# Kernel tuning notes

Measured on AMD Instinct MI355X. Metric: run time of the kernel, lower is better.

Reference implementation:

```python
import jax, jax.numpy as jnp
from jax import lax
import numpy as np

B, S, E, HID = 16, 7, 64, 64
RES = (64, 64); D = RES[0] * RES[1]
XLOW, XHIGH = -0.5, 0.5
RLOW, RHIGH = float(np.sqrt(0.01)), float(np.sqrt(0.05))
PIXEL_MULT = 1.0; N_ITER = 3; TSOFT = 1.0 / float(np.sqrt(E))

def _build_grid():
    ranges = [np.linspace(XLOW, XHIGH, r) for r in RES]
    g = np.stack(np.meshgrid(*ranges, indexing='xy'), axis=-1)
    g = g.reshape(RES[0], RES[1], -1).reshape(1, -1, 2)
    return jnp.asarray(g, dtype=jnp.float32)

ABS_GRID = _build_grid()  # [1, D, 2]

def _ln(x, g, b):
    m = jnp.mean(x, -1, keepdims=True)
    v = jnp.mean(jnp.square(x - m), -1, keepdims=True)
    return (x - m) * lax.rsqrt(v + 1e-5) * g + b

def _forward(data, slot_noise, pos_rand, conv0_w, conv0_b, conv1_w, conv1_b, conv2_w, conv2_b,
             dataN_g, dataN_b, queryN_g, queryN_b, toK_w, toK_b, toV_w, toV_b, dense_w, dense_b,
             mlp1_w, mlp1_b, mlp2_w, mlp2_b, gru_wih, gru_whh, gru_bih, gru_bhh,
             alpha1_w, alpha1_b, alpha2_w, alpha2_b, final1_w, final1_b, final2_w, final2_b,
             slots_mu, slots_logsigma):
    dn = ('NCHW', 'OIHW', 'NCHW')
    def conv(x, w, b):
        return lax.conv_general_dilated(x, w, (1, 1), 'SAME', dimension_numbers=dn) + b[None, :, None, None]
    # CNN encoder: Conv-ReLU x3, 'same' padding, k=5
    x = jax.nn.relu(conv(data, conv0_w, conv0_b))
    x = jax.nn.relu(conv(x, conv1_w, conv1_b))
    x = jax.nn.relu(conv(x, conv2_w, conv2_b))
    enc = x.transpose(0, 2, 3, 1).reshape(B, D, HID)
    enc = _ln(enc, dataN_g, dataN_b)

    queries = slots_mu + jnp.exp(slots_logsigma) * slot_noise  # [B,S,E]
    # init_slots: faithful replication (source indexes the SLOT dim, and swaps rlow/rhigh)
    pos_scale = pos_rand.at[:, :2, :].add(-0.5)
    pos_scale = pos_scale.at[:, -1, :].set((RLOW - RHIGH) * pos_rand[:, -1, :] + RHIGH)

    encK = enc @ toK_w + toK_b  # [B,D,E]
    encV = enc @ toV_w + toV_b

    def init_mlp(y):
        y = _ln(y, queryN_g, queryN_b)
        return jax.nn.relu(y @ mlp1_w + mlp1_b) @ mlp2_w + mlp2_b

    def get_kv(ps):
        # per-slot relative grid: [B,S,D,2]
        rel = (ABS_GRID[:, None] - ps[:, :, None, :2]) / ps[:, :, -1][:, :, None, None]
        eg = PIXEL_MULT * (rel @ dense_w + dense_b)  # [B,S,D,E]
        return init_mlp(encK[:, None] + eg), init_mlp(encV[:, None] + eg)

    def att_wts(q, k):
        logits = jnp.einsum('bse,bsde->bsd', q, k) * TSOFT
        att = jax.nn.softmax(logits, axis=1)  # softmax over slots
        wts = att / jnp.sum(att, -1, keepdims=True) + 1e-8
        return att, wts

    def update_frames(wts):
        new_pos = jnp.einsum('bsd,de->bse', wts, ABS_GRID[0])  # [B,S,2]
        d2 = jnp.sum(jnp.square(ABS_GRID[:, None] - new_pos[:, :, None]), -1)  # [B,S,D]
        new_scale = jnp.sqrt(jnp.einsum('bsd,bsd->bs', wts, d2))
        return jnp.concatenate([new_pos, new_scale[..., None]], -1)

    def gru(xg, h):
        gi = xg @ gru_wih.T + gru_bih
        gh = h @ gru_whh.T + gru_bhh
        ir, iz, inn = jnp.split(gi, 3, -1)
        hr, hz, hn = jnp.split(gh, 3, -1)
        r = jax.nn.sigmoid(ir + hr)
        z = jax.nn.sigmoid(iz + hz)
        n = jnp.tanh(inn + r * hn)
        return (1.0 - z) * n + z * h

    for _ in range(N_ITER):
        keys, vals = get_kv(pos_scale)
        att, wts = att_wts(_ln(queries, queryN_g, queryN_b), keys)
        pos_scale = update_frames(wts)
        upd = jnp.einsum('bsd,bsde->bse', wts, vals)
        queries = gru(upd.reshape(-1, E), queries.reshape(-1, E)).reshape(B, S, E)

    keys, _ = get_kv(pos_scale)
    att, wts = att_wts(_ln(queries, queryN_g, queryN_b), keys)
    nps = update_frames(wts)
    alpha = jax.nn.sigmoid(jax.nn.relu(queries @ alpha1_w + alpha1_b) @ alpha2_w + alpha2_b)
    slot_feat = jax.nn.relu(queries @ final1_w + final1_b) @ final2_w + final2_b + nps
    return queries, att, slot_feat, alpha

def setup_inputs() -> dict:
    ks = jax.random.split(jax.random.key(0), 20)
    f32 = jnp.float32
    def rn(i, shape, s):
        return jax.random.normal(ks[i], shape, f32) * s
    inp = dict(
        data=jax.random.normal(ks[0], (B, 1, RES[0], RES[1]), f32),
        slot_noise=jax.random.normal(ks[1], (B, S, E), f32),
        pos_rand=jax.random.uniform(ks[2], (B, S, 3), dtype=f32),
        conv0_w=rn(3, (HID, 1, 5, 5), 0.2), conv0_b=jnp.zeros(HID, f32),
        conv1_w=rn(4, (HID, HID, 5, 5), 0.025), conv1_b=jnp.zeros(HID, f32),
        conv2_w=rn(5, (HID, HID, 5, 5), 0.025), conv2_b=jnp.zeros(HID, f32),
        dataN_g=jnp.ones(HID, f32), dataN_b=jnp.zeros(HID, f32),
        queryN_g=jnp.ones(E, f32), queryN_b=jnp.zeros(E, f32),
        toK_w=rn(6, (HID, E), 0.125), toK_b=jnp.zeros(E, f32),
        toV_w=rn(7, (HID, E), 0.125), toV_b=jnp.zeros(E, f32),
        dense_w=rn(8, (2, E), 0.7), dense_b=jnp.zeros(E, f32),
        mlp1_w=rn(9, (E, E), 0.125), mlp1_b=jnp.zeros(E, f32),
        mlp2_w=rn(10, (E, E), 0.125), mlp2_b=jnp.zeros(E, f32),
        gru_wih=rn(11, (3 * E, E), 0.125), gru_whh=rn(12, (3 * E, E), 0.125),
        gru_bih=jnp.zeros(3 * E, f32), gru_bhh=jnp.zeros(3 * E, f32),
        alpha1_w=rn(13, (E, 32), 0.125), alpha1_b=jnp.zeros(32, f32),
        alpha2_w=rn(14, (32, 1), 0.18), alpha2_b=jnp.zeros(1, f32),
        final1_w=rn(15, (E, HID), 0.125), final1_b=jnp.zeros(HID, f32),
        final2_w=rn(16, (HID, 3), 0.125), final2_b=jnp.zeros(3, f32),
        slots_mu=rn(17, (1, 1, E), 1.0),
        slots_logsigma=rn(18, (1, 1, E), 0.01),
    )
    return inp

def reference(data, slot_noise, pos_rand, conv0_w, conv0_b, conv1_w, conv1_b, conv2_w, conv2_b,
              dataN_g, dataN_b, queryN_g, queryN_b, toK_w, toK_b, toV_w, toV_b, dense_w, dense_b,
              mlp1_w, mlp1_b, mlp2_w, mlp2_b, gru_wih, gru_whh, gru_bih, gru_bhh,
              alpha1_w, alpha1_b, alpha2_w, alpha2_b, final1_w, final1_b, final2_w, final2_b,
              slots_mu, slots_logsigma):
    return _forward(data, slot_noise, pos_rand, conv0_w, conv0_b, conv1_w, conv1_b, conv2_w, conv2_b,
                    dataN_g, dataN_b, queryN_g, queryN_b, toK_w, toK_b, toV_w, toV_b, dense_w, dense_b,
                    mlp1_w, mlp1_b, mlp2_w, mlp2_b, gru_wih, gru_whh, gru_bih, gru_bhh,
                    alpha1_w, alpha1_b, alpha2_w, alpha2_b, final1_w, final1_b, final2_w, final2_b,
                    slots_mu, slots_logsigma)
```

## Files before the change

kernel.cpp:

```cpp
#include <hip/hip_runtime.h>
#include <cmath>


#define RLOW_F 0.1f
#define RHIGH_F 0.22360679774997896f
#define W0CONST 1.00004096f
#define SR2 704.3386243f

typedef __attribute__((ext_vector_type(8))) __bf16 bf16x8;
typedef __attribute__((ext_vector_type(4))) float f32x4;

__device__ __forceinline__ float wsum64(float v){
  #pragma unroll
  for (int off = 32; off > 0; off >>= 1) v += __shfl_xor(v, off, 64);
  return v;
}
__device__ __forceinline__ float rdlane(float v, int l){
  return __int_as_float(__builtin_amdgcn_readlane(__float_as_int(v), l));
}
__device__ __forceinline__ unsigned short bf16bits(float v){
  __bf16 h = (__bf16)v;
  return *reinterpret_cast<unsigned short*>(&h);
}

__device__ __forceinline__ void pp_core(int row, int e, float qv,
    float px, float py, float sc,
    const float* __restrict__ qg_, const float* __restrict__ qb_,
    const float* __restrict__ dw, const float* __restrict__ db,
    const float* __restrict__ mlp2w, const float* __restrict__ mlp2b,
    float* __restrict__ absc, float* __restrict__ w2qc){
  float m = wsum64(qv) * (1.f/64.f);
  float d = qv - m;
  float var = wsum64(d*d) * (1.f/64.f);
  float qlnv = d * (1.0f/sqrtf(var + 1e-5f)) * qg_[e] + qb_[e];
  float A  = dw[e]      / sc;
  float Bv = dw[64 + e] / sc;
  absc[row*192 + e]       = A;
  absc[row*192 + 64 + e]  = Bv;
  absc[row*192 + 128 + e] = db[e] - px*A - py*Bv;
  float acc = 0.f;
  const float* wrow = mlp2w + e*64;
  for (int j = 0; j < 64; j++) acc = fmaf(wrow[j], rdlane(qlnv, j), acc);
  w2qc[row*68 + e] = acc;
  float c2 = wsum64(mlp2b[e] * qlnv);
  if (e == 0) w2qc[row*68 + 64] = c2;
}

__global__ void k_prep(const float* __restrict__ noise, const float* __restrict__ prand,
                       const float* __restrict__ mu, const float* __restrict__ logsig,
                       const float* __restrict__ qg_, const float* __restrict__ qb_,
                       const float* __restrict__ dw, const float* __restrict__ db,
                       const float* __restrict__ mlp2w, const float* __restrict__ mlp2b,
                       float* __restrict__ queries, float* __restrict__ ps,
                       float* __restrict__ absc, float* __restrict__ w2qc,
                       float* __restrict__ accF, float* __restrict__ upd){
  int row = blockIdx.x;
  int e = threadIdx.x;
  int s = row % 7;
  float qv = mu[e] + expf(logsig[e]) * noise[row*64 + e];
  queries[row*64 + e] = qv;
  upd[row*64 + e] = 0.f;
  if (e < 4) accF[row*4 + e] = 0.f;
  float pv = 0.f;
  if (e < 3){
    float pr = prand[row*3 + e];
    if (s < 2)       pv = pr - 0.5f;
    else if (s == 6) pv = (RLOW_F - RHIGH_F)*pr + RHIGH_F;
    else             pv = pr;
    ps[row*3 + e] = pv;
  }
  float px = rdlane(pv, 0), py = rdlane(pv, 1), sc = rdlane(pv, 2);
  pp_core(row, e, qv, px, py, sc, qg_, qb_, dw, db, mlp2w, mlp2b, absc, w2qc);
}

__global__ __launch_bounds__(256) void k_conv0(const float* __restrict__ in,
                        const float* __restrict__ w, const float* __restrict__ bias,
                        unsigned short* __restrict__ out){
  int bi = blockIdx.x; int b = bi >> 6; int y = bi & 63;
  int t = threadIdx.x; int lane = t & 63; int xg = t >> 6;
  __shared__ float s_in[5*68];
  __shared__ float s_w[64*25];
  __shared__ float s_out[64*65];
  for (int i = t; i < 1600; i += 256) s_w[i] = w[i];
  for (int i = t; i < 340; i += 256){
    int r = i / 68, cx = i % 68;
    int yy = y + r - 2, gx = cx - 2;
    float v = 0.f;
    if (yy >= 0 && yy < 64 && gx >= 0 && gx < 64) v = in[(b*64 + yy)*64 + gx];
    s_in[r*68 + cx] = v;
  }
  __syncthreads();
  int o = lane;
  float bvv = bias[o];
  float acc[16];
  #pragma unroll
  for (int k = 0; k < 16; k++) acc[k] = bvv;
  #pragma unroll
  for (int ky = 0; ky < 5; ky++){
    float rv[20];
    const float4* p = reinterpret_cast<const float4*>(&s_in[ky*68 + xg*16]);
    #pragma unroll
    for (int q = 0; q < 5; q++){ float4 f = p[q]; rv[q*4]=f.x; rv[q*4+1]=f.y; rv[q*4+2]=f.z; rv[q*4+3]=f.w; }
    #pragma unroll
    for (int kx = 0; kx < 5; kx++){
      float wv = s_w[o*25 + ky*5 + kx];
      #pragma unroll
      for (int k = 0; k < 16; k++) acc[k] = fmaf(rv[k+kx], wv, acc[k]);
    }
  }
  #pragma unroll
  for (int k = 0; k < 16; k++) s_out[o*65 + xg*16 + k] = fmaxf(acc[k], 0.f);
  __syncthreads();
  for (int i = t; i < 4096; i += 256){
    int px = i >> 6, ch = i & 63;
    out[((size_t)(b*64 + y)*64 + px)*64 + ch] = bf16bits(s_out[ch*65 + px]);
  }
}

__global__ void k_packconv(const float* __restrict__ w, unsigned short* __restrict__ out){
  int idx = blockIdx.x*256 + threadIdx.x;
  if (idx >= 102400) return;
  int j = idx & 7;
  int l = (idx >> 3) & 63;
  int frag = idx >> 9;
  int nt = frag & 3;
  int ks = (frag >> 2) % 10;
  int dy = frag / 40;
  int q = l >> 4, cr = l & 15;
  int k = ks*32 + q*8 + j;
  int kx = k >> 6, ch = k & 63;
  int n = nt*16 + cr;
  out[idx] = bf16bits(w[((n*64 + ch)*5 + dy)*5 + kx]);
}

__global__ __launch_bounds__(256) void k_convm(const unsigned short* __restrict__ in_bf,
                        const unsigned short* __restrict__ wpack,
                        const float* __restrict__ bias,
                        const float* __restrict__ lng, const float* __restrict__ lnb,
                        unsigned short* __restrict__ out_bf, float* __restrict__ out_f,
                        int mode){
  int bi = blockIdx.x;
  int b = bi >> 4; int yg = bi & 15;
  int t = threadIdx.x; int wv = t >> 6; int l = t & 63;
  int q = l >> 4, cr = l & 15;
  int p0 = wv*16;

  __shared__ char lds[8*68*144];

  for (int ri = 0; ri < 8; ri++){
    int yy = yg*4 + ri - 2;
    bool rok = (yy >= 0 && yy < 64);
    const uint4* src = reinterpret_cast<const uint4*>(in_bf + (size_t)(b*64 + yy)*64*64);
    for (int i = t; i < 544; i += 256){
      int px = i >> 3, c8 = i & 7;
      uint4 v = {0u,0u,0u,0u};
      int gx = px - 2;
      if (rok && gx >= 0 && gx < 64) v = src[gx*8 + c8];
      *reinterpret_cast<uint4*>(&lds[ri*9792 + px*144 + c8*16]) = v;
    }
  }
  __syncthreads();

  f32x4 acc[4][4];
  #pragma unroll
  for (int r = 0; r < 4; r++)
    #pragma unroll
    for (int nt = 0; nt < 4; nt++) acc[r][nt] = (f32x4){0.f,0.f,0.f,0.f};

  const bf16x8* wp = reinterpret_cast<const bf16x8*>(wpack);
  for (int dy = 0; dy < 5; dy++){
    for (int ks = 0; ks < 10; ks++){
      bf16x8 Bf[4];
      int fbase = (dy*10 + ks)*4;
      #pragma unroll
      for (int nt = 0; nt < 4; nt++) Bf[nt] = wp[(fbase + nt)*64 + l];
      int aoff = (p0 + cr + (ks >> 1))*144 + (ks & 1)*64 + q*16;
      #pragma unroll
      for (int r = 0; r < 4; r++){
        bf16x8 a = *reinterpret_cast<const bf16x8*>(&lds[(r + dy)*9792 + aoff]);
        #pragma unroll
        for (int nt = 0; nt < 4; nt++)
          acc[r][nt] = __builtin_amdgcn_mfma_f32_16x16x32_bf16(a, Bf[nt], acc[r][nt], 0, 0, 0);
      }
    }
  }

  float bvv[4];
  #pragma unroll
  for (int nt = 0; nt < 4; nt++) bvv[nt] = bias[nt*16 + cr];

  if (mode == 0){
    #pragma unroll
    for (int r = 0; r < 4; r++){
      int y = yg*4 + r;
      #pragma unroll
      for (int reg = 0; reg < 4; reg++){
        int p = p0 + q*4 + reg;
        size_t base = ((size_t)(b*64 + y)*64 + p)*64;
        #pragma unroll
        for (int nt = 0; nt < 4; nt++)
          out_bf[base + nt*16 + cr] = bf16bits(fmaxf(acc[r][nt][reg] + bvv[nt], 0.f));
      }
    }
  } else {
    float gv[4], bb[4];
    #pragma unroll
    for (int nt = 0; nt < 4; nt++){ gv[nt] = lng[nt*16 + cr]; bb[nt] = lnb[nt*16 + cr]; }
    #pragma unroll
    for (int r = 0; r < 4; r++){
      int y = yg*4 + r;
      #pragma unroll
      for (int reg = 0; reg < 4; reg++){
        int p = p0 + q*4 + reg;
        float v[4]; float s1 = 0.f, s2 = 0.f;
        #pragma unroll
        for (int nt = 0; nt < 4; nt++){
          v[nt] = fmaxf(acc[r][nt][reg] + bvv[nt], 0.f);
          s1 += v[nt]; s2 += v[nt]*v[nt];
        }
        #pragma unroll
        for (int m = 1; m < 16; m <<= 1){ s1 += __shfl_xor(s1, m, 64); s2 += __shfl_xor(s2, m, 64); }
        float mean = s1 * (1.f/64.f);
        float var  = s2 * (1.f/64.f) - mean*mean;
        float rstd = 1.0f/sqrtf(var + 1e-5f);
        size_t base = ((size_t)b*4096 + y*64 + p)*64;
        #pragma unroll
        for (int nt = 0; nt < 4; nt++)
          out_f[base + nt*16 + cr] = (v[nt] - mean)*rstd*gv[nt] + bb[nt];
      }
    }
  }
}

__global__ void k_packw1(const float* __restrict__ w1, unsigned short* __restrict__ out){
  int idx = blockIdx.x*256 + threadIdx.x;
  int jj = idx & 7;
  int lane = (idx >> 3) & 63;
  int frag = idx >> 9;
  int ks = frag >> 2, nt = frag & 3;
  int q = lane >> 4, cr = lane & 15;
  int k = ks*32 + q*8 + jj;
  int n = nt*16 + cr;
  out[idx] = bf16bits(w1[k*64 + n]);
}

__global__ __launch_bounds__(256) void k_projm(const float* __restrict__ enc,
                       const unsigned short* __restrict__ kpack, const float* __restrict__ bk,
                       const unsigned short* __restrict__ vpack, const float* __restrict__ bvp,
                       unsigned short* __restrict__ K, unsigned short* __restrict__ V){
  int bi = blockIdx.x; int b = bi >> 6; int tile = bi & 63;
  int t = threadIdx.x; int wv = t >> 6; int l = t & 63;
  int q = l >> 4, cr = l & 15;
  int d0 = tile*64 + wv*16;

  const bf16x8* kp = reinterpret_cast<const bf16x8*>(kpack);
  const bf16x8* vp = reinterpret_cast<const bf16x8*>(vpack);
  bf16x8 KB[8], VB[8];
  #pragma unroll
  for (int f = 0; f < 8; f++){ KB[f] = kp[f*64 + l]; VB[f] = vp[f*64 + l]; }

  const float* er = enc + (size_t)(b*4096 + d0 + cr)*64;
  bf16x8 a0, a1;
  #pragma unroll
  for (int h = 0; h < 2; h++){
    const float4* e4 = reinterpret_cast<const float4*>(er + (h ? (32 + q*8) : (q*8)));
    #pragma unroll
    for (int p = 0; p < 2; p++){
      float4 e = e4[p];
      if (h == 0){ a0[p*4+0]=(__bf16)e.x; a0[p*4+1]=(__bf16)e.y; a0[p*4+2]=(__bf16)e.z; a0[p*4+3]=(__bf16)e.w; }
      else       { a1[p*4+0]=(__bf16)e.x; a1[p*4+1]=(__bf16)e.y; a1[p*4+2]=(__bf16)e.z; a1[p*4+3]=(__bf16)e.w; }
    }
  }

  f32x4 zero = {0.f,0.f,0.f,0.f};
  f32x4 aK[4], aV[4];
  #pragma unroll
  for (int nt = 0; nt < 4; nt++){
    aK[nt] = __builtin_amdgcn_mfma_f32_16x16x32_bf16(a0, KB[nt],     zero,   0, 0, 0);
    aK[nt] = __builtin_amdgcn_mfma_f32_16x16x32_bf16(a1, KB[4 + nt], aK[nt], 0, 0, 0);
    aV[nt] = __builtin_amdgcn_mfma_f32_16x16x32_bf16(a0, VB[nt],     zero,   0, 0, 0);
    aV[nt] = __builtin_amdgcn_mfma_f32_16x16x32_bf16(a1, VB[4 + nt], aV[nt], 0, 0, 0);
  }
  #pragma unroll
  for (int nt = 0; nt < 4; nt++){
    float bkv = bk[nt*16 + cr], bvv = bvp[nt*16 + cr];
    #pragma unroll
    for (int reg = 0; reg < 4; reg++){
      size_t base = ((size_t)b*4096 + d0 + q*4 + reg)*64 + nt*16 + cr;
      K[base] = bf16bits(aK[nt][reg] + bkv);
      V[base] = bf16bits(aV[nt][reg] + bvv);
    }
  }
}

__global__ __launch_bounds__(256) void k_attnK(const unsigned short* __restrict__ encX,
     const unsigned short* __restrict__ w1pack, const float* __restrict__ mlp1b,
     const float* __restrict__ absc, const float* __restrict__ qg_,
     const float* __restrict__ qb_, const float* __restrict__ w2qc,
     float* __restrict__ att, float* __restrict__ accF){
  int bi = blockIdx.x;
  int b = bi >> 6, tile = bi & 63;
  int t = threadIdx.x; int wv = t >> 6; int l = t & 63;
  int q = l >> 4, cr = l & 15;
  int m0 = tile*64 + wv*16;
  int drow = m0 + cr;

  __shared__ float s_log[7*64];
  __shared__ float s_absc[7*192];
  __shared__ float s_wq[7*68];
  for (int i = t; i < 1344; i += 256) s_absc[i] = absc[b*7*192 + i];
  for (int i = t; i < 476;  i += 256) s_wq[i]   = w2qc[b*7*68 + i];

  const bf16x8* wp = reinterpret_cast<const bf16x8*>(w1pack);
  bf16x8 Bf[8];
  #pragma unroll
  for (int f = 0; f < 8; f++) Bf[f] = wp[f*64 + l];

  const unsigned short* er = encX + (size_t)(b*4096 + drow)*64;
  float gx = -0.5f + (float)(drow & 63) * (1.f/63.f);
  float gy = -0.5f + (float)((drow >> 6) & 63) * (1.f/63.f);
  float xb[16], gq[16], bq[16];
  {
    bf16x8 ea = *reinterpret_cast<const bf16x8*>(er + q*8);
    bf16x8 eb = *reinterpret_cast<const bf16x8*>(er + 32 + q*8);
    #pragma unroll
    for (int i = 0; i < 8; i++){ xb[i] = (float)ea[i]; xb[8+i] = (float)eb[i]; }
  }
  #pragma unroll
  for (int h = 0; h < 2; h++){
    int fb = h ? (32 + q*8) : (q*8);
    const float4* g4 = reinterpret_cast<const float4*>(qg_ + fb);
    const float4* b4 = reinterpret_cast<const float4*>(qb_ + fb);
    #pragma unroll
    for (int p = 0; p < 2; p++){
      float4 gg = g4[p], bb = b4[p];
      int o = h*8 + p*4;
      gq[o+0]=gg.x; gq[o+1]=gg.y; gq[o+2]=gg.z; gq[o+3]=gg.w;
      bq[o+0]=bb.x; bq[o+1]=bb.y; bq[o+2]=bb.z; bq[o+3]=bb.w;
    }
  }
  float b1v[4];
  #pragma unroll
  for (int nt = 0; nt < 4; nt++) b1v[nt] = mlp1b[nt*16 + cr];
  __syncthreads();

  for (int s = 0; s < 7; s++){
    const float* Ac = s_absc + s*192;
    float x[16];
    #pragma unroll
    for (int h = 0; h < 2; h++){
      int fb = h ? (32 + q*8) : (q*8);
      const float4* A4 = reinterpret_cast<const float4*>(Ac + fb);
      const float4* B4 = reinterpret_cast<const float4*>(Ac + 64 + fb);
      const float4* C4 = reinterpret_cast<const float4*>(Ac + 128 + fb);
      #pragma unroll
      for (int p = 0; p < 2; p++){
        float4 Av = A4[p], Bv = B4[p], Cv = C4[p];
        int o = h*8 + p*4;
        x[o+0] = xb[o+0] + gx*Av.x + gy*Bv.x + Cv.x;
        x[o+1] = xb[o+1] + gx*Av.y + gy*Bv.y + Cv.y;
        x[o+2] = xb[o+2] + gx*Av.z + gy*Bv.z + Cv.z;
        x[o+3] = xb[o+3] + gx*Av.w + gy*Bv.w + Cv.w;
      }
    }
    float sum = 0.f;
    #pragma unroll
    for (int k = 0; k < 16; k++) sum += x[k];
    sum += __shfl_xor(sum, 16, 64); sum += __shfl_xor(sum, 32, 64);
    float m = sum * (1.f/64.f);
    float v = 0.f;
    #pragma unroll
    for (int k = 0; k < 16; k++){ float dd = x[k] - m; v += dd*dd; }
    v += __shfl_xor(v, 16, 64); v += __shfl_xor(v, 32, 64);
    float rstd = 1.0f/sqrtf(v * (1.f/64.f) + 1e-5f);

    bf16x8 a0, a1;
    #pragma unroll
    for (int k = 0; k < 8; k++)  a0[k] = (__bf16)((x[k]   - m)*rstd*gq[k]   + bq[k]);
    #pragma unroll
    for (int k = 0; k < 8; k++)  a1[k] = (__bf16)((x[8+k] - m)*rstd*gq[8+k] + bq[8+k]);

    f32x4 zero = {0.f, 0.f, 0.f, 0.f};
    f32x4 acc[4];
    #pragma unroll
    for (int nt = 0; nt < 4; nt++){
      acc[nt] = __builtin_amdgcn_mfma_f32_16x16x32_bf16(a0, Bf[nt],     zero,    0, 0, 0);
      acc[nt] = __builtin_amdgcn_mfma_f32_16x16x32_bf16(a1, Bf[4 + nt], acc[nt], 0, 0, 0);
    }

    float c2 = s_wq[s*68 + 64];
    float p[4] = {0.f, 0.f, 0.f, 0.f};
    #pragma unroll
    for (int nt = 0; nt < 4; nt++){
      float wqv = s_wq[s*68 + nt*16 + cr];
      #pragma unroll
      for (int reg = 0; reg < 4; reg++){
        float y = fmaxf(acc[nt][reg] + b1v[nt], 0.f);
        p[reg] = fmaf(y, wqv, p[reg]);
      }
    }
    #pragma unroll
    for (int reg = 0; reg < 4; reg++){
      #pragma unroll
      for (int off = 1; off < 16; off <<= 1) p[reg] += __shfl_xor(p[reg], off, 64);
    }
    if (cr == 0){
      #pragma unroll
      for (int reg = 0; reg < 4; reg++)
        s_log[s*64 + wv*16 + q*4 + reg] = (p[reg] + c2) * 0.125f;
    }
  }
  __syncthreads();

  if (t < 64){
    float lv[7];
    #pragma unroll
    for (int s = 0; s < 7; s++) lv[s] = s_log[s*64 + t];
    float mx = lv[0];
    #pragma unroll
    for (int s = 1; s < 7; s++) mx = fmaxf(mx, lv[s]);
    float sm = 0.f;
    #pragma unroll
    for (int s = 0; s < 7; s++){ lv[s] = expf(lv[s] - mx); sm += lv[s]; }
    float inv = 1.0f / sm;
    #pragma unroll
    for (int s = 0; s < 7; s++){
      float a = lv[s] * inv;
      s_log[s*64 + t] = a;
      att[(size_t)(b*7+s)*4096 + tile*64 + t] = a;
    }
  }
  __syncthreads();

  if (t < 224){
    int s = t >> 5, r = t & 31;
    float a1 = s_log[s*64 + r];
    float a2 = s_log[s*64 + r + 32];
    float gx1 = -0.5f + (float)r * (1.f/63.f);
    float gx2 = -0.5f + (float)(r + 32) * (1.f/63.f);
    float gyc = -0.5f + (float)tile * (1.f/63.f);
    float gy2c = gyc*gyc;
    float w0 = a1 + a2;
    float w1 = a1*gx1 + a2*gx2;
    float w2 = w0*gyc;
    float w3 = a1*(gx1*gx1 + gy2c) + a2*(gx2*gx2 + gy2c);
    #pragma unroll
    for (int m = 1; m < 32; m <<= 1){
      w0 += __shfl_xor(w0, m, 64);
      w1 += __shfl_xor(w1, m, 64);
      w2 += __shfl_xor(w2, m, 64);
      w3 += __shfl_xor(w3, m, 64);
    }
    if (r == 0){
      atomicAdd(&accF[(b*7+s)*4 + 0], w0);
      atomicAdd(&accF[(b*7+s)*4 + 1], w1);
      atomicAdd(&accF[(b*7+s)*4 + 2], w2);
      atomicAdd(&accF[(b*7+s)*4 + 3], w3);
    }
  }
}

__global__ __launch_bounds__(256) void k_attnV(const unsigned short* __restrict__ encX,
     const unsigned short* __restrict__ w1pack, const float* __restrict__ mlp1b,
     const float* __restrict__ absc, const float* __restrict__ qg_,
     const float* __restrict__ qb_, const float* __restrict__ att,
     const float* __restrict__ accF, float* __restrict__ upd){
  int bi = blockIdx.x;
  int b = bi >> 6, tile = bi & 63;
  int t = threadIdx.x; int wv = t >> 6; int l = t & 63;
  int q = l >> 4, cr = l & 15;
  int m0 = tile*64 + wv*16;
  int drow = m0 + cr;

  __shared__ float s_absc[7*192];
  __shared__ float s_att[7*64];
  __shared__ float s_upd[7*64];
  __shared__ float s_inv[7];
  for (int i = t; i < 1344; i += 256) s_absc[i] = absc[b*7*192 + i];
  for (int i = t; i < 448;  i += 256){
    s_att[i] = att[(size_t)(b*7 + (i >> 6))*4096 + tile*64 + (i & 63)];
    s_upd[i] = 0.f;
  }
  if (t < 7) s_inv[t] = 1.0f / accF[(b*7 + t)*4];

  const bf16x8* wp = reinterpret_cast<const bf16x8*>(w1pack);
  bf16x8 Bf[8];
  #pragma unroll
  for (int f = 0; f < 8; f++) Bf[f] = wp[f*64 + l];

  const unsigned short* er = encX + (size_t)(b*4096 + drow)*64;
  float gx = -0.5f + (float)(drow & 63) * (1.f/63.f);
  float gy = -0.5f + (float)((drow >> 6) & 63) * (1.f/63.f);
  float xb[16], gq[16], bq[16];
  {
    bf16x8 ea = *reinterpret_cast<const bf16x8*>(er + q*8);
    bf16x8 eb = *reinterpret_cast<const bf16x8*>(er + 32 + q*8);
    #pragma unroll
    for (int i = 0; i < 8; i++){ xb[i] = (float)ea[i]; xb[8+i] = (float)eb[i]; }
  }
  #pragma unroll
  for (int h = 0; h < 2; h++){
    int fb = h ? (32 + q*8) : (q*8);
    const float4* g4 = reinterpret_cast<const float4*>(qg_ + fb);
    const float4* b4 = reinterpret_cast<const float4*>(qb_ + fb);
    #pragma unroll
    for (int p = 0; p < 2; p++){
      float4 gg = g4[p], bb = b4[p];
      int o = h*8 + p*4;
      gq[o+0]=gg.x; gq[o+1]=gg.y; gq[o+2]=gg.z; gq[o+3]=gg.w;
      bq[o+0]=bb.x; bq[o+1]=bb.y; bq[o+2]=bb.z; bq[o+3]=bb.w;
    }
  }
  float b1v[4];
  #pragma unroll
  for (int nt = 0; nt < 4; nt++) b1v[nt] = mlp1b[nt*16 + cr];
  __syncthreads();

  for (int s = 0; s < 7; s++){
    const float* Ac = s_absc + s*192;
    float x[16];
    #pragma unroll
    for (int h = 0; h < 2; h++){
      int fb = h ? (32 + q*8) : (q*8);
      const float4* A4 = reinterpret_cast<const float4*>(Ac + fb);
      const float4* B4 = reinterpret_cast<const float4*>(Ac + 64 + fb);
      const float4* C4 = reinterpret_cast<const float4*>(Ac + 128 + fb);
      #pragma unroll
      for (int p = 0; p < 2; p++){
        float4 Av = A4[p], Bv = B4[p], Cv = C4[p];
        int o = h*8 + p*4;
        x[o+0] = xb[o+0] + gx*Av.x + gy*Bv.x + Cv.x;
        x[o+1] = xb[o+1] + gx*Av.y + gy*Bv.y + Cv.y;
        x[o+2] = xb[o+2] + gx*Av.z + gy*Bv.z + Cv.z;
        x[o+3] = xb[o+3] + gx*Av.w + gy*Bv.w + Cv.w;
      }
    }
    float sum = 0.f;
    #pragma unroll
    for (int k = 0; k < 16; k++) sum += x[k];
    sum += __shfl_xor(sum, 16, 64); sum += __shfl_xor(sum, 32, 64);
    float m = sum * (1.f/64.f);
    float v = 0.f;
    #pragma unroll
    for (int k = 0; k < 16; k++){ float dd = x[k] - m; v += dd*dd; }
    v += __shfl_xor(v, 16, 64); v += __shfl_xor(v, 32, 64);
    float rstd = 1.0f/sqrtf(v * (1.f/64.f) + 1e-5f);

    bf16x8 a0, a1;
    #pragma unroll
    for (int k = 0; k < 8; k++)  a0[k] = (__bf16)((x[k]   - m)*rstd*gq[k]   + bq[k]);
    #pragma unroll
    for (int k = 0; k < 8; k++)  a1[k] = (__bf16)((x[8+k] - m)*rstd*gq[8+k] + bq[8+k]);

    f32x4 zero = {0.f, 0.f, 0.f, 0.f};
    f32x4 acc[4];
    #pragma unroll
    for (int nt = 0; nt < 4; nt++){
      acc[nt] = __builtin_amdgcn_mfma_f32_16x16x32_bf16(a0, Bf[nt],     zero,    0, 0, 0);
      acc[nt] = __builtin_amdgcn_mfma_f32_16x16x32_bf16(a1, Bf[4 + nt], acc[nt], 0, 0, 0);
    }

    float rsa = s_inv[s];
    float wr[4];
    #pragma unroll
    for (int reg = 0; reg < 4; reg++)
      wr[reg] = fmaf(s_att[s*64 + wv*16 + q*4 + reg], rsa, 1e-8f);
    float pc[4];
    #pragma unroll
    for (int nt = 0; nt < 4; nt++){
      pc[nt] = 0.f;
      #pragma unroll
      for (int reg = 0; reg < 4; reg++)
        pc[nt] = fmaf(wr[reg], fmaxf(acc[nt][reg] + b1v[nt], 0.f), pc[nt]);
    }
    #pragma unroll
    for (int nt = 0; nt < 4; nt++){
      pc[nt] += __shfl_xor(pc[nt], 16, 64);
      pc[nt] += __shfl_xor(pc[nt], 32, 64);
    }
    if (q == 0){
      #pragma unroll
      for (int nt = 0; nt < 4; nt++)
        atomicAdd(&s_upd[s*64 + nt*16 + cr], pc[nt]);
    }
  }
  __syncthreads();
  for (int i = t; i < 448; i += 256)
    atomicAdd(&upd[b*448 + i], s_upd[i]);
}

__global__ void k_gru(float* __restrict__ upd, float* __restrict__ queries,
                      const float* __restrict__ wih, const float* __restrict__ whh,
                      const float* __restrict__ bih, const float* __restrict__ bhh,
                      const float* __restrict__ mlp2w, const float* __restrict__ mlp2b,
                      float* __restrict__ accF, float* __restrict__ ps,
                      const float* __restrict__ qg_, const float* __restrict__ qb_,
                      const float* __restrict__ dw, const float* __restrict__ db,
                      float* __restrict__ absc, float* __restrict__ w2qc){
  int row = blockIdx.x; int t = threadIdx.x;
  __shared__ float us[64], hs[64], xs[64], gis[192], ghs[192];
  __shared__ float s_ps3[3];
  if (t < 64){ us[t] = upd[row*64 + t]; hs[t] = queries[row*64 + t]; }
  if (t == 64){
    float sa = accF[row*4+0];
    float ax = accF[row*4+1], ay = accF[row*4+2], ar2 = accF[row*4+3];
    float isa = 1.0f/sa;
    float Wx = ax*isa, Wy = ay*isa;
    float Wg = ar2*isa + 1e-8f*SR2;
    float s2 = Wg - (Wx*Wx + Wy*Wy)*(2.f - W0CONST);
    s_ps3[0] = Wx; s_ps3[1] = Wy; s_ps3[2] = sqrtf(fmaxf(s2, 0.f));
  }
  __syncthreads();
  if (t < 64){
    float a = W0CONST * mlp2b[t];
    for (int i = 0; i < 64; i++) a = fmaf(us[i], mlp2w[i*64 + t], a);
    xs[t] = a;
  }
  __syncthreads();
  float gi = bih[t], gh = bhh[t];
  for (int e = 0; e < 64; e++){
    gi = fmaf(wih[t*64 + e], xs[e], gi);
    gh = fmaf(whh[t*64 + e], hs[e], gh);
  }
  gis[t] = gi; ghs[t] = gh;
  __syncthreads();
  if (t < 64){
    float r = 1.0f/(1.0f + expf(-(gis[t]      + ghs[t])));
    float z = 1.0f/(1.0f + expf(-(gis[64+t]   + ghs[64+t])));
    float n = tanhf(gis[128+t] + r*ghs[128+t]);
    float newq = (1.0f - z)*n + z*hs[t];
    queries[row*64 + t] = newq;
    upd[row*64 + t] = 0.f;
    if (t < 4) accF[row*4 + t] = 0.f;
    if (t < 3) ps[row*3 + t] = s_ps3[t];
    pp_core(row, t, newq, s_ps3[0], s_ps3[1], s_ps3[2],
            qg_, qb_, dw, db, mlp2w, mlp2b, absc, w2qc);
  }
}

__global__ void k_final(const float* __restrict__ queries, const float* __restrict__ accF,
                        const float* __restrict__ a1w, const float* __restrict__ a1b,
                        const float* __restrict__ a2w, const float* __restrict__ a2b,
                        const float* __restrict__ f1w, const float* __restrict__ f1b,
                        const float* __restrict__ f2w, const float* __restrict__ f2b,
                        float* __restrict__ out){
  int bs = blockIdx.x; int e = threadIdx.x;
  __shared__ float qs[64], hf[64], ha[32];
  float q = queries[bs*64 + e];
  qs[e] = q;
  out[bs*64 + e] = q;
  __syncthreads();
  float accf = f1b[e];
  for (int i = 0; i < 64; i++) accf = fmaf(qs[i], f1w[i*64 + e], accf);
  hf[e] = fmaxf(accf, 0.f);
  if (e < 32){
    float acca = a1b[e];
    for (int i = 0; i < 64; i++) acca = fmaf(qs[i], a1w[i*32 + e], acca);
    ha[e] = fmaxf(acca, 0.f);
  }
  __syncthreads();
  if (e < 3){
    float sf = f2b[e];
    for (int o = 0; o < 64; o++) sf = fmaf(hf[o], f2w[o*3 + e], sf);
    float sa = accF[bs*4+0], ax = accF[bs*4+1], ay = accF[bs*4+2], ar2 = accF[bs*4+3];
    float isa = 1.0f/sa;
    float Wx = ax*isa, Wy = ay*isa;
    float Wg = ar2*isa + 1e-8f*SR2;
    float s2 = Wg - (Wx*Wx + Wy*Wy)*(2.f - W0CONST);
    float nv = (e == 0) ? Wx : ((e == 1) ? Wy : sqrtf(fmaxf(s2, 0.f)));
    out[465920 + bs*3 + e] = sf + nv;
  }
  if (e == 32){
    float al = a2b[0];
    for (int o = 0; o < 32; o++) al = fmaf(ha[o], a2w[o], al);
    out[466256 + bs] = 1.0f/(1.0f + expf(-al));
  }
}

extern "C" void kernel_launch(void* const* d_in, const int* in_sizes, int n_in,
                              void* d_out, int out_size, void* d_ws, size_t ws_size,
                              hipStream_t stream){
  const float* data        = (const float*)d_in[0];
  const float* slot_noise  = (const float*)d_in[1];
  const float* pos_rand    = (const float*)d_in[2];
  const float* conv0_w     = (const float*)d_in[3];
  const float* conv0_b     = (const float*)d_in[4];
  const float* conv1_w     = (const float*)d_in[5];
  const float* conv1_b     = (const float*)d_in[6];
  const float* conv2_w     = (const float*)d_in[7];
  const float* conv2_b     = (const float*)d_in[8];
  const float* dataN_g     = (const float*)d_in[9];
  const float* dataN_b     = (const float*)d_in[10];
  const float* queryN_g    = (const float*)d_in[11];
  const float* queryN_b    = (const float*)d_in[12];
  const float* toK_w       = (const float*)d_in[13];
  const float* toK_b       = (const float*)d_in[14];
  const float* toV_w       = (const float*)d_in[15];
  const float* toV_b       = (const float*)d_in[16];
  const float* dense_w     = (const float*)d_in[17];
  const float* dense_b     = (const float*)d_in[18];
  const float* mlp1_w      = (const float*)d_in[19];
  const float* mlp1_b      = (const float*)d_in[20];
  const float* mlp2_w      = (const float*)d_in[21];
  const float* mlp2_b      = (const float*)d_in[22];
  const float* gru_wih     = (const float*)d_in[23];
  const float* gru_whh     = (const float*)d_in[24];
  const float* gru_bih     = (const float*)d_in[25];
  const float* gru_bhh     = (const float*)d_in[26];
  const float* alpha1_w    = (const float*)d_in[27];
  const float* alpha1_b    = (const float*)d_in[28];
  const float* alpha2_w    = (const float*)d_in[29];
  const float* alpha2_b    = (const float*)d_in[30];
  const float* final1_w    = (const float*)d_in[31];
  const float* final1_b    = (const float*)d_in[32];
  const float* final2_w    = (const float*)d_in[33];
  const float* final2_b    = (const float*)d_in[34];
  const float* slots_mu    = (const float*)d_in[35];
  const float* slots_lsig  = (const float*)d_in[36];

  float* ws   = (float*)d_ws;
  float* bufA = ws;
  float* bufB = bufA + 4194304;
  float* bufC = bufB + 4194304;
  float* attw = bufC + 4194304;
  float* queries = attw + 458752;
  float* ps   = queries + 7168;
  float* absc = ps + 512;
  float* accF = absc + 21504;
  float* upd  = accF + 512;
  float* w2qc = upd + 7168;
  unsigned short* w1pack = (unsigned short*)(w2qc + 7616);
  unsigned short* kpack  = w1pack + 4096;
  unsigned short* vpack  = kpack + 4096;
  unsigned short* wp1    = vpack + 4096;
  unsigned short* wp2    = wp1 + 102400;

  unsigned short* c0_bf = (unsigned short*)bufA;
  unsigned short* c1_bf = (unsigned short*)bufC;
  float* enc = bufB;
  unsigned short* encK = (unsigned short*)bufA;
  unsigned short* encV = (unsigned short*)bufC;

  float* outq   = (float*)d_out;
  float* outatt = outq + 7168;

  k_prep<<<112, 64, 0, stream>>>(slot_noise, pos_rand, slots_mu, slots_lsig,
                                 queryN_g, queryN_b, dense_w, dense_b, mlp2_w, mlp2_b,
                                 queries, ps, absc, w2qc, accF, upd);
  k_packw1<<<16, 256, 0, stream>>>(mlp1_w, w1pack);
  k_packw1<<<16, 256, 0, stream>>>(toK_w, kpack);
  k_packw1<<<16, 256, 0, stream>>>(toV_w, vpack);
  k_packconv<<<400, 256, 0, stream>>>(conv1_w, wp1);
  k_packconv<<<400, 256, 0, stream>>>(conv2_w, wp2);
  k_conv0<<<1024, 256, 0, stream>>>(data, conv0_w, conv0_b, c0_bf);
  k_convm<<<256, 256, 0, stream>>>(c0_bf, wp1, conv1_b, nullptr, nullptr, c1_bf, nullptr, 0);
  k_convm<<<256, 256, 0, stream>>>(c1_bf, wp2, conv2_b, dataN_g, dataN_b, nullptr, enc, 1);
  k_projm<<<1024, 256, 0, stream>>>(enc, kpack, toK_b, vpack, toV_b, encK, encV);

  for (int p = 0; p < 4; p++){
    float* attp = (p == 3) ? outatt : attw;
    k_attnK<<<1024, 256, 0, stream>>>(encK, w1pack, mlp1_b, absc, queryN_g, queryN_b,
                                      w2qc, attp, accF);
    if (p < 3){
      k_attnV<<<1024, 256, 0, stream>>>(encV, w1pack, mlp1_b, absc, queryN_g, queryN_b,
                                        attp, accF, upd);
      k_gru<<<112, 192, 0, stream>>>(upd, queries, gru_wih, gru_whh, gru_bih, gru_bhh,
                                     mlp2_w, mlp2_b, accF, ps, queryN_g, queryN_b,
                                     dense_w, dense_b, absc, w2qc);
    }
  }
  k_final<<<112, 64, 0, stream>>>(queries, accF,
                                  alpha1_w, alpha1_b, alpha2_w, alpha2_b,
                                  final1_w, final1_b, final2_w, final2_b, outq);
}
```

Before: 535.2 us.

## Fuse attention-K and attention-V kernels with deferred normalization and partitioned accumulators

The separate key-logit and value-update kernels become one kernel. It computes the softmax attention per tile and, in the same launch, accumulates the weighted value MLP outputs. The per-slot attention normalization (divide by total attention mass) is moved into the GRU kernel by keeping two partial sums, the attention-weighted sum and the plain sum for the epsilon term. This removes the intermediate attention buffer round-trip and one launch per iteration. Tiles shrink to 32 rows, with slots split across wave pairs for more blocks, and global atomics are spread over 4 partition buffers to reduce contention. The cost is extra shared-memory atomics and partial-sum traffic.

```diff
diff --git a/kernel.cpp b/kernel.cpp
--- a/kernel.cpp
+++ b/kernel.cpp
@@ -53,14 +53,14 @@
                        const float* __restrict__ mlp2w, const float* __restrict__ mlp2b,
                        float* __restrict__ queries, float* __restrict__ ps,
                        float* __restrict__ absc, float* __restrict__ w2qc,
-                       float* __restrict__ accF, float* __restrict__ upd){
+                       float* __restrict__ accF, float* __restrict__ gpbuf){
   int row = blockIdx.x;
   int e = threadIdx.x;
   int s = row % 7;
   float qv = mu[e] + expf(logsig[e]) * noise[row*64 + e];
   queries[row*64 + e] = qv;
-  upd[row*64 + e] = 0.f;
   if (e < 4) accF[row*4 + e] = 0.f;
+  for (int i = row*64 + e; i < 57344; i += 7168) gpbuf[i] = 0.f;
   float pv = 0.f;
   if (e < 3){
     float pr = prand[row*3 + e];
@@ -293,39 +293,42 @@
   }
 }
 
-__global__ __launch_bounds__(256) void k_attnK(const unsigned short* __restrict__ encX,
+__global__ __launch_bounds__(256) void k_attn(
+     const unsigned short* __restrict__ encK, const unsigned short* __restrict__ encV,
      const unsigned short* __restrict__ w1pack, const float* __restrict__ mlp1b,
      const float* __restrict__ absc, const float* __restrict__ qg_,
      const float* __restrict__ qb_, const float* __restrict__ w2qc,
-     float* __restrict__ att, float* __restrict__ accF){
+     float* __restrict__ accF, float* __restrict__ gp1P, float* __restrict__ gp2P,
+     float* __restrict__ att_out, int mode){
   int bi = blockIdx.x;
-  int b = bi >> 6, tile = bi & 63;
+  int b = bi >> 7, tile = bi & 127;
   int t = threadIdx.x; int wv = t >> 6; int l = t & 63;
   int q = l >> 4, cr = l & 15;
-  int m0 = tile*64 + wv*16;
+  int rg = wv & 1, sg = wv >> 1;
+  int m0 = tile*32 + rg*16;
   int drow = m0 + cr;
-
-  __shared__ float s_log[7*64];
+  int sbeg = sg*4, send = sg ? 7 : 4;
+
+  __shared__ float s_log[7*32];
   __shared__ float s_absc[7*192];
   __shared__ float s_wq[7*68];
-  for (int i = t; i < 1344; i += 256) s_absc[i] = absc[b*7*192 + i];
-  for (int i = t; i < 476;  i += 256) s_wq[i]   = w2qc[b*7*68 + i];
+  __shared__ float s_up1[7*64];
+  __shared__ float s_up2[7*64];
+
+  for (int i = t; i < 1344; i += 256) s_absc[i] = absc[b*1344 + i];
+  for (int i = t; i < 476;  i += 256) s_wq[i]   = w2qc[b*476 + i];
+  if (mode == 0){
+    for (int i = t; i < 448; i += 256){ s_up1[i] = 0.f; s_up2[i] = 0.f; }
+  }
 
   const bf16x8* wp = reinterpret_cast<const bf16x8*>(w1pack);
   bf16x8 Bf[8];
   #pragma unroll
   for (int f = 0; f < 8; f++) Bf[f] = wp[f*64 + l];
 
-  const unsigned short* er = encX + (size_t)(b*4096 + drow)*64;
   float gx = -0.5f + (float)(drow & 63) * (1.f/63.f);
   float gy = -0.5f + (float)((drow >> 6) & 63) * (1.f/63.f);
-  float xb[16], gq[16], bq[16];
-  {
-    bf16x8 ea = *reinterpret_cast<const bf16x8*>(er + q*8);
-    bf16x8 eb = *reinterpret_cast<const bf16x8*>(er + 32 + q*8);
-    #pragma unroll
-    for (int i = 0; i < 8; i++){ xb[i] = (float)ea[i]; xb[8+i] = (float)eb[i]; }
-  }
+  float gq[16], bq[16];
   #pragma unroll
   for (int h = 0; h < 2; h++){
     int fb = h ? (32 + q*8) : (q*8);
@@ -342,9 +345,18 @@
   float b1v[4];
   #pragma unroll
   for (int nt = 0; nt < 4; nt++) b1v[nt] = mlp1b[nt*16 + cr];
-  __syncthreads();
-
-  for (int s = 0; s < 7; s++){
+
+  float xb[16];
+  {
+    const unsigned short* er = encK + (size_t)(b*4096 + drow)*64;
+    bf16x8 ea = *reinterpret_cast<const bf16x8*>(er + q*8);
+    bf16x8 eb = *reinterpret_cast<const bf16x8*>(er + 32 + q*8);
+    #pragma unroll
+    for (int i = 0; i < 8; i++){ xb[i] = (float)ea[i]; xb[8+i] = (float)eb[i]; }
+  }
+  __syncthreads();
+
+  for (int s = sbeg; s < send; s++){
     const float* Ac = s_absc + s*192;
     float x[16];
     #pragma unroll
@@ -407,15 +419,15 @@
     if (cr == 0){
       #pragma unroll
       for (int reg = 0; reg < 4; reg++)
-        s_log[s*64 + wv*16 + q*4 + reg] = (p[reg] + c2) * 0.125f;
-    }
-  }
-  __syncthreads();
-
-  if (t < 64){
+        s_log[s*32 + rg*16 + q*4 + reg] = (p[reg] + c2) * 0.125f;
+    }
+  }
+  __syncthreads();
+
+  if (t < 32){
     float lv[7];
     #pragma unroll
-    for (int s = 0; s < 7; s++) lv[s] = s_log[s*64 + t];
+    for (int s = 0; s < 7; s++) lv[s] = s_log[s*32 + t];
     float mx = lv[0];
     #pragma unroll
     for (int s = 1; s < 7; s++) mx = fmaxf(mx, lv[s]);
@@ -426,24 +438,19 @@
     #pragma unroll
     for (int s = 0; s < 7; s++){
       float a = lv[s] * inv;
-      s_log[s*64 + t] = a;
-      att[(size_t)(b*7+s)*4096 + tile*64 + t] = a;
+      s_log[s*32 + t] = a;
+      if (mode == 1) att_out[(size_t)(b*7+s)*4096 + tile*32 + t] = a;
     }
   }
   __syncthreads();
 
   if (t < 224){
     int s = t >> 5, r = t & 31;
-    float a1 = s_log[s*64 + r];
-    float a2 = s_log[s*64 + r + 32];
-    float gx1 = -0.5f + (float)r * (1.f/63.f);
-    float gx2 = -0.5f + (float)(r + 32) * (1.f/63.f);
-    float gyc = -0.5f + (float)tile * (1.f/63.f);
-    float gy2c = gyc*gyc;
-    float w0 = a1 + a2;
-    float w1 = a1*gx1 + a2*gx2;
-    float w2 = w0*gyc;
-    float w3 = a1*(gx1*gx1 + gy2c) + a2*(gx2*gx2 + gy2c);
+    float a = s_log[s*32 + r];
+    int d = tile*32 + r;
+    float gxr = -0.5f + (float)(d & 63) * (1.f/63.f);
+    float gyr = -0.5f + (float)(d >> 6) * (1.f/63.f);
+    float w0 = a, w1 = a*gxr, w2 = a*gyr, w3 = a*(gxr*gxr + gyr*gyr);
     #pragma unroll
     for (int m = 1; m < 32; m <<= 1){
       w0 += __shfl_xor(w0, m, 64);
@@ -458,138 +465,103 @@
       atomicAdd(&accF[(b*7+s)*4 + 3], w3);
     }
   }
-}
-
-__global__ __launch_bounds__(256) void k_attnV(const unsigned short* __restrict__ encX,
-     const unsigned short* __restrict__ w1pack, const float* __restrict__ mlp1b,
-     const float* __restrict__ absc, const float* __restrict__ qg_,
-     const float* __restrict__ qb_, const float* __restrict__ att,
-     const float* __restrict__ accF, float* __restrict__ upd){
-  int bi = blockIdx.x;
-  int b = bi >> 6, tile = bi & 63;
-  int t = threadIdx.x; int wv = t >> 6; int l = t & 63;
-  int q = l >> 4, cr = l & 15;
-  int m0 = tile*64 + wv*16;
-  int drow = m0 + cr;
-
-  __shared__ float s_absc[7*192];
-  __shared__ float s_att[7*64];
-  __shared__ float s_upd[7*64];
-  __shared__ float s_inv[7];
-  for (int i = t; i < 1344; i += 256) s_absc[i] = absc[b*7*192 + i];
-  for (int i = t; i < 448;  i += 256){
-    s_att[i] = att[(size_t)(b*7 + (i >> 6))*4096 + tile*64 + (i & 63)];
-    s_upd[i] = 0.f;
-  }
-  if (t < 7) s_inv[t] = 1.0f / accF[(b*7 + t)*4];
-
-  const bf16x8* wp = reinterpret_cast<const bf16x8*>(w1pack);
-  bf16x8 Bf[8];
-  #pragma unroll
-  for (int f = 0; f < 8; f++) Bf[f] = wp[f*64 + l];
-
-  const unsigned short* er = encX + (size_t)(b*4096 + drow)*64;
-  float gx = -0.5f + (float)(drow & 63) * (1.f/63.f);
-  float gy = -0.5f + (float)((drow >> 6) & 63) * (1.f/63.f);
-  float xb[16], gq[16], bq[16];
-  {
-    bf16x8 ea = *reinterpret_cast<const bf16x8*>(er + q*8);
-    bf16x8 eb = *reinterpret_cast<const bf16x8*>(er + 32 + q*8);
-    #pragma unroll
-    for (int i = 0; i < 8; i++){ xb[i] = (float)ea[i]; xb[8+i] = (float)eb[i]; }
-  }
-  #pragma unroll
-  for (int h = 0; h < 2; h++){
-    int fb = h ? (32 + q*8) : (q*8);
-    const float4* g4 = reinterpret_cast<const float4*>(qg_ + fb);
-    const float4* b4 = reinterpret_cast<const float4*>(qb_ + fb);
-    #pragma unroll
-    for (int p = 0; p < 2; p++){
-      float4 gg = g4[p], bb = b4[p];
-      int o = h*8 + p*4;
-      gq[o+0]=gg.x; gq[o+1]=gg.y; gq[o+2]=gg.z; gq[o+3]=gg.w;
-      bq[o+0]=bb.x; bq[o+1]=bb.y; bq[o+2]=bb.z; bq[o+3]=bb.w;
-    }
-  }
-  float b1v[4];
-  #pragma unroll
-  for (int nt = 0; nt < 4; nt++) b1v[nt] = mlp1b[nt*16 + cr];
-  __syncthreads();
-
-  for (int s = 0; s < 7; s++){
-    const float* Ac = s_absc + s*192;
-    float x[16];
-    #pragma unroll
-    for (int h = 0; h < 2; h++){
-      int fb = h ? (32 + q*8) : (q*8);
-      const float4* A4 = reinterpret_cast<const float4*>(Ac + fb);
-      const float4* B4 = reinterpret_cast<const float4*>(Ac + 64 + fb);
-      const float4* C4 = reinterpret_cast<const float4*>(Ac + 128 + fb);
-      #pragma unroll
-      for (int p = 0; p < 2; p++){
-        float4 Av = A4[p], Bv = B4[p], Cv = C4[p];
-        int o = h*8 + p*4;
-        x[o+0] = xb[o+0] + gx*Av.x + gy*Bv.x + Cv.x;
-        x[o+1] = xb[o+1] + gx*Av.y + gy*Bv.y + Cv.y;
-        x[o+2] = xb[o+2] + gx*Av.z + gy*Bv.z + Cv.z;
-        x[o+3] = xb[o+3] + gx*Av.w + gy*Bv.w + Cv.w;
-      }
-    }
-    float sum = 0.f;
-    #pragma unroll
-    for (int k = 0; k < 16; k++) sum += x[k];
-    sum += __shfl_xor(sum, 16, 64); sum += __shfl_xor(sum, 32, 64);
-    float m = sum * (1.f/64.f);
-    float v = 0.f;
-    #pragma unroll
-    for (int k = 0; k < 16; k++){ float dd = x[k] - m; v += dd*dd; }
-    v += __shfl_xor(v, 16, 64); v += __shfl_xor(v, 32, 64);
-    float rstd = 1.0f/sqrtf(v * (1.f/64.f) + 1e-5f);
-
-    bf16x8 a0, a1;
-    #pragma unroll
-    for (int k = 0; k < 8; k++)  a0[k] = (__bf16)((x[k]   - m)*rstd*gq[k]   + bq[k]);
-    #pragma unroll
-    for (int k = 0; k < 8; k++)  a1[k] = (__bf16)((x[8+k] - m)*rstd*gq[8+k] + bq[8+k]);
-
-    f32x4 zero = {0.f, 0.f, 0.f, 0.f};
-    f32x4 acc[4];
-    #pragma unroll
-    for (int nt = 0; nt < 4; nt++){
-      acc[nt] = __builtin_amdgcn_mfma_f32_16x16x32_bf16(a0, Bf[nt],     zero,    0, 0, 0);
-      acc[nt] = __builtin_amdgcn_mfma_f32_16x16x32_bf16(a1, Bf[4 + nt], acc[nt], 0, 0, 0);
-    }
-
-    float rsa = s_inv[s];
-    float wr[4];
-    #pragma unroll
-    for (int reg = 0; reg < 4; reg++)
-      wr[reg] = fmaf(s_att[s*64 + wv*16 + q*4 + reg], rsa, 1e-8f);
-    float pc[4];
-    #pragma unroll
-    for (int nt = 0; nt < 4; nt++){
-      pc[nt] = 0.f;
+
+  if (mode == 0){
+    float vb[16];
+    {
+      const unsigned short* er = encV + (size_t)(b*4096 + drow)*64;
+      bf16x8 ea = *reinterpret_cast<const bf16x8*>(er + q*8);
+      bf16x8 eb = *reinterpret_cast<const bf16x8*>(er + 32 + q*8);
+      #pragma unroll
+      for (int i = 0; i < 8; i++){ vb[i] = (float)ea[i]; vb[8+i] = (float)eb[i]; }
+    }
+    for (int s = sbeg; s < send; s++){
+      const float* Ac = s_absc + s*192;
+      float x[16];
+      #pragma unroll
+      for (int h = 0; h < 2; h++){
+        int fb = h ? (32 + q*8) : (q*8);
+        const float4* A4 = reinterpret_cast<const float4*>(Ac + fb);
+        const float4* B4 = reinterpret_cast<const float4*>(Ac + 64 + fb);
+        const float4* C4 = reinterpret_cast<const float4*>(Ac + 128 + fb);
+        #pragma unroll
+        for (int p = 0; p < 2; p++){
+          float4 Av = A4[p], Bv = B4[p], Cv = C4[p];
+          int o = h*8 + p*4;
+          x[o+0] = vb[o+0] + gx*Av.x + gy*Bv.x + Cv.x;
+          x[o+1] = vb[o+1] + gx*Av.y + gy*Bv.y + Cv.y;
+          x[o+2] = vb[o+2] + gx*Av.z + gy*Bv.z + Cv.z;
+          x[o+3] = vb[o+3] + gx*Av.w + gy*Bv.w + Cv.w;
+        }
+      }
+      float sum = 0.f;
+      #pragma unroll
+      for (int k = 0; k < 16; k++) sum += x[k];
+      sum += __shfl_xor(sum, 16, 64); sum += __shfl_xor(sum, 32, 64);
+      float m = sum * (1.f/64.f);
+      float v = 0.f;
+      #pragma unroll
+      for (int k = 0; k < 16; k++){ float dd = x[k] - m; v += dd*dd; }
+      v += __shfl_xor(v, 16, 64); v += __shfl_xor(v, 32, 64);
+      float rstd = 1.0f/sqrtf(v * (1.f/64.f) + 1e-5f);
+
+      bf16x8 a0, a1;
+      #pragma unroll
+      for (int k = 0; k < 8; k++)  a0[k] = (__bf16)((x[k]   - m)*rstd*gq[k]   + bq[k]);
+      #pragma unroll
+      for (int k = 0; k < 8; k++)  a1[k] = (__bf16)((x[8+k] - m)*rstd*gq[8+k] + bq[8+k]);
+
+      f32x4 zero = {0.f, 0.f, 0.f, 0.f};
+      f32x4 acc[4];
+      #pragma unroll
+      for (int nt = 0; nt < 4; nt++){
+        acc[nt] = __builtin_amdgcn_mfma_f32_16x16x32_bf16(a0, Bf[nt],     zero,    0, 0, 0);
+        acc[nt] = __builtin_amdgcn_mfma_f32_16x16x32_bf16(a1, Bf[4 + nt], acc[nt], 0, 0, 0);
+      }
+
+      float wr[4];
       #pragma unroll
       for (int reg = 0; reg < 4; reg++)
-        pc[nt] = fmaf(wr[reg], fmaxf(acc[nt][reg] + b1v[nt], 0.f), pc[nt]);
-    }
-    #pragma unroll
-    for (int nt = 0; nt < 4; nt++){
-      pc[nt] += __shfl_xor(pc[nt], 16, 64);
-      pc[nt] += __shfl_xor(pc[nt], 32, 64);
-    }
-    if (q == 0){
-      #pragma unroll
-      for (int nt = 0; nt < 4; nt++)
-        atomicAdd(&s_upd[s*64 + nt*16 + cr], pc[nt]);
-    }
-  }
-  __syncthreads();
-  for (int i = t; i < 448; i += 256)
-    atomicAdd(&upd[b*448 + i], s_upd[i]);
-}
-
-__global__ void k_gru(float* __restrict__ upd, float* __restrict__ queries,
+        wr[reg] = s_log[s*32 + rg*16 + q*4 + reg];
+      float pc1[4], pc2[4];
+      #pragma unroll
+      for (int nt = 0; nt < 4; nt++){
+        pc1[nt] = 0.f; pc2[nt] = 0.f;
+        #pragma unroll
+        for (int reg = 0; reg < 4; reg++){
+          float y = fmaxf(acc[nt][reg] + b1v[nt], 0.f);
+          pc1[nt] = fmaf(wr[reg], y, pc1[nt]);
+          pc2[nt] += y;
+        }
+      }
+      #pragma unroll
+      for (int nt = 0; nt < 4; nt++){
+        pc1[nt] += __shfl_xor(pc1[nt], 16, 64);
+        pc1[nt] += __shfl_xor(pc1[nt], 32, 64);
+        pc2[nt] += __shfl_xor(pc2[nt], 16, 64);
+        pc2[nt] += __shfl_xor(pc2[nt], 32, 64);
+      }
+      if (q == 0){
+        #pragma unroll
+        for (int nt = 0; nt < 4; nt++){
+          atomicAdd(&s_up1[s*64 + nt*16 + cr], pc1[nt]);
+          atomicAdd(&s_up2[s*64 + nt*16 + cr], pc2[nt]);
+        }
+      }
+    }
+    __syncthreads();
+    int part = tile & 3;
+    float* g1 = gp1P + part*7168 + b*448;
+    float* g2 = gp2P + part*7168 + b*448;
+    for (int i = t; i < 448; i += 256){
+      atomicAdd(&g1[i], s_up1[i]);
+      atomicAdd(&g2[i], s_up2[i]);
+    }
+  }
+}
+
+__global__ void k_gru(float* __restrict__ gp1P, float* __restrict__ gp2P,
+                      float* __restrict__ queries,
                       const float* __restrict__ wih, const float* __restrict__ whh,
                       const float* __restrict__ bih, const float* __restrict__ bhh,
                       const float* __restrict__ mlp2w, const float* __restrict__ mlp2b,
@@ -600,7 +572,20 @@
   int row = blockIdx.x; int t = threadIdx.x;
   __shared__ float us[64], hs[64], xs[64], gis[192], ghs[192];
   __shared__ float s_ps3[3];
-  if (t < 64){ us[t] = upd[row*64 + t]; hs[t] = queries[row*64 + t]; }
+  if (t < 64){
+    float sa = accF[row*4 + 0];
+    float isa = 1.0f/sa;
+    float g1 = 0.f, g2 = 0.f;
+    #pragma unroll
+    for (int p = 0; p < 4; p++){
+      g1 += gp1P[p*7168 + row*64 + t];
+      g2 += gp2P[p*7168 + row*64 + t];
+      gp1P[p*7168 + row*64 + t] = 0.f;
+      gp2P[p*7168 + row*64 + t] = 0.f;
+    }
+    us[t] = g1*isa + 1e-8f*g2;
+    hs[t] = queries[row*64 + t];
+  }
   if (t == 64){
     float sa = accF[row*4+0];
     float ax = accF[row*4+1], ay = accF[row*4+2], ar2 = accF[row*4+3];
@@ -630,7 +615,6 @@
     float n = tanhf(gis[128+t] + r*ghs[128+t]);
     float newq = (1.0f - z)*n + z*hs[t];
     queries[row*64 + t] = newq;
-    upd[row*64 + t] = 0.f;
     if (t < 4) accF[row*4 + t] = 0.f;
     if (t < 3) ps[row*3 + t] = s_ps3[t];
     pp_core(row, t, newq, s_ps3[0], s_ps3[1], s_ps3[2],
@@ -722,13 +706,13 @@
   float* bufA = ws;
   float* bufB = bufA + 4194304;
   float* bufC = bufB + 4194304;
-  float* attw = bufC + 4194304;
-  float* queries = attw + 458752;
+  float* queries = bufC + 4194304;
   float* ps   = queries + 7168;
   float* absc = ps + 512;
   float* accF = absc + 21504;
-  float* upd  = accF + 512;
-  float* w2qc = upd + 7168;
+  float* gp1P = accF + 512;
+  float* gp2P = gp1P + 28672;
+  float* w2qc = gp2P + 28672;
   unsigned short* w1pack = (unsigned short*)(w2qc + 7616);
   unsigned short* kpack  = w1pack + 4096;
   unsigned short* vpack  = kpack + 4096;
@@ -746,7 +730,7 @@
 
   k_prep<<<112, 64, 0, stream>>>(slot_noise, pos_rand, slots_mu, slots_lsig,
                                  queryN_g, queryN_b, dense_w, dense_b, mlp2_w, mlp2_b,
-                                 queries, ps, absc, w2qc, accF, upd);
+                                 queries, ps, absc, w2qc, accF, gp1P);
   k_packw1<<<16, 256, 0, stream>>>(mlp1_w, w1pack);
   k_packw1<<<16, 256, 0, stream>>>(toK_w, kpack);
   k_packw1<<<16, 256, 0, stream>>>(toV_w, vpack);
@@ -757,18 +741,18 @@
   k_convm<<<256, 256, 0, stream>>>(c1_bf, wp2, conv2_b, dataN_g, dataN_b, nullptr, enc, 1);
   k_projm<<<1024, 256, 0, stream>>>(enc, kpack, toK_b, vpack, toV_b, encK, encV);
 
-  for (int p = 0; p < 4; p++){
-    float* attp = (p == 3) ? outatt : attw;
-    k_attnK<<<1024, 256, 0, stream>>>(encK, w1pack, mlp1_b, absc, queryN_g, queryN_b,
-                                      w2qc, attp, accF);
-    if (p < 3){
-      k_attnV<<<1024, 256, 0, stream>>>(encV, w1pack, mlp1_b, absc, queryN_g, queryN_b,
-                                        attp, accF, upd);
-      k_gru<<<112, 192, 0, stream>>>(upd, queries, gru_wih, gru_whh, gru_bih, gru_bhh,
-                                     mlp2_w, mlp2_b, accF, ps, queryN_g, queryN_b,
-                                     dense_w, dense_b, absc, w2qc);
-    }
-  }
+  for (int p = 0; p < 3; p++){
+    k_attn<<<2048, 256, 0, stream>>>(encK, encV, w1pack, mlp1_b, absc,
+                                     queryN_g, queryN_b, w2qc,
+                                     accF, gp1P, gp2P, outatt, 0);
+    k_gru<<<112, 192, 0, stream>>>(gp1P, gp2P, queries,
+                                   gru_wih, gru_whh, gru_bih, gru_bhh,
+                                   mlp2_w, mlp2_b, accF, ps, queryN_g, queryN_b,
+                                   dense_w, dense_b, absc, w2qc);
+  }
+  k_attn<<<2048, 256, 0, stream>>>(encK, encV, w1pack, mlp1_b, absc,
+                                   queryN_g, queryN_b, w2qc,
+                                   accF, gp1P, gp2P, outatt, 1);
   k_final<<<112, 64, 0, stream>>>(queries, accF,
                                   alpha1_w, alpha1_b, alpha2_w, alpha2_b,
                                   final1_w, final1_b, final2_w, final2_b, outq);
```

Measured after the change: 681.2 us. 27.3% more time.
